# Kernel optimization log

Hardware: AMD Instinct MI355X
Metric: run time of the kernel (lower is better)

The kernel has to match this reference:

```python
import math
import jax
import jax.numpy as jnp
import numpy as np

NUM_TOKENS = 8192
MODEL_DIM = 2048
NUM_EXPERTS = 64
CAPACITY_FACTOR = 1.0


def setup_inputs() -> dict:
    key = jax.random.key(0)
    k1, k2 = jax.random.split(key)
    x = jax.random.normal(k1, (NUM_TOKENS, MODEL_DIM), dtype=jnp.float32)
    # gate weight, torch Linear layout [num_experts, model_dim]
    wg = jax.random.normal(k2, (NUM_EXPERTS, MODEL_DIM), dtype=jnp.float32) / np.sqrt(MODEL_DIM).astype(np.float32)
    return {"x": x, "wg": wg}


def top2gating(logits, capacity_factor):
    s, e = logits.shape  # static under jit
    capacity = int(math.ceil(2 * s / e * capacity_factor))
    gates = jax.nn.softmax(logits, axis=1)  # [s, e]

    # top-1 expert
    indices1_s = jnp.argmax(gates, axis=1)
    mask1 = jax.nn.one_hot(indices1_s, e, dtype=jnp.int32)  # [s, e]

    # top-2 expert via gumbel-perturbed logits with expert-1 masked out
    gumbel = jax.random.gumbel(jax.random.key(42), logits.shape, dtype=logits.dtype)
    logits_w_noise = logits + gumbel
    logits_except1 = jnp.where(mask1.astype(bool), -jnp.inf, logits_w_noise)
    indices2_s = jnp.argmax(logits_except1, axis=1)
    mask2 = jax.nn.one_hot(indices2_s, e, dtype=jnp.int32)

    # positions within each expert's buffer (prefix sums over tokens)
    locations1 = jnp.cumsum(mask1, axis=0) - 1  # [s, e]
    locations2 = jnp.cumsum(mask2, axis=0) - 1
    locations2 = locations2 + jnp.sum(mask1, axis=0, keepdims=True)

    # load-balancing aux loss
    me = jnp.mean(gates, axis=0)
    ce = jnp.mean(mask1.astype(gates.dtype), axis=0)
    l_aux = jnp.mean(me * ce) * (e * e)

    # drop tokens beyond capacity
    mask1 = mask1 * (locations1 < capacity).astype(jnp.int32)
    mask2 = mask2 * (locations2 < capacity).astype(jnp.int32)

    locations1_s = jnp.sum(locations1 * mask1, axis=1)  # [s]
    locations2_s = jnp.sum(locations2 * mask2, axis=1)

    mask1_f = mask1.astype(gates.dtype)
    mask2_f = mask2.astype(gates.dtype)
    gates1_s = jnp.sum(gates * mask1_f, axis=1)  # [s]
    gates2_s = jnp.sum(gates * mask2_f, axis=1)
    denom_s = jnp.maximum(gates1_s + gates2_s, jnp.finfo(gates.dtype).eps)
    gates1_s = gates1_s / denom_s
    gates2_s = gates2_s / denom_s

    gates1 = gates1_s[:, None] * mask1_f  # [s, e]
    gates2 = gates2_s[:, None] * mask2_f

    locations1_sc = jax.nn.one_hot(locations1_s, capacity, dtype=gates.dtype)  # [s, c]
    locations2_sc = jax.nn.one_hot(locations2_s, capacity, dtype=gates.dtype)

    combine_weights = (gates1[:, :, None] * locations1_sc[:, None, :]
                       + gates2[:, :, None] * locations2_sc[:, None, :])  # [s, e, c]
    dispatch_mask = combine_weights.astype(bool)
    return l_aux, combine_weights, dispatch_mask


def reference(x, wg):
    logits = x @ wg.T  # [s, e]
    return top2gating(logits, CAPACITY_FACTOR)
```

## Files before the change

### kernel.cpp

```cpp
#include <hip/hip_runtime.h>
#include <hip/hip_bf16.h>
#include <stdint.h>

#define TOKENS 8192
#define DIM 2048
#define EXPERTS 64
#define CAP 256
#define COMB_ELEMS ((size_t)TOKENS * EXPERTS * CAP)
#define OUT_ELEMS (1 + 2 * COMB_ELEMS)

__device__ __forceinline__ void tf_round(uint32_t& a, uint32_t& b, int r) {
  a += b;
  b = (b << r) | (b >> (32 - r));
  b ^= a;
}

__device__ __forceinline__ void threefry2x32(uint32_t k0, uint32_t k1,
                                             uint32_t x0, uint32_t x1,
                                             uint32_t& o0, uint32_t& o1) {
  const uint32_t ks0 = k0, ks1 = k1, ks2 = k0 ^ k1 ^ 0x1BD11BDAu;
  x0 += ks0; x1 += ks1;
  tf_round(x0, x1, 13); tf_round(x0, x1, 15); tf_round(x0, x1, 26); tf_round(x0, x1, 6);
  x0 += ks1; x1 += ks2 + 1u;
  tf_round(x0, x1, 17); tf_round(x0, x1, 29); tf_round(x0, x1, 16); tf_round(x0, x1, 24);
  x0 += ks2; x1 += ks0 + 2u;
  tf_round(x0, x1, 13); tf_round(x0, x1, 15); tf_round(x0, x1, 26); tf_round(x0, x1, 6);
  x0 += ks0; x1 += ks1 + 3u;
  tf_round(x0, x1, 17); tf_round(x0, x1, 29); tf_round(x0, x1, 16); tf_round(x0, x1, 24);
  x0 += ks1; x1 += ks2 + 4u;
  tf_round(x0, x1, 13); tf_round(x0, x1, 15); tf_round(x0, x1, 26); tf_round(x0, x1, 6);
  x0 += ks2; x1 += ks0 + 5u;
  o0 = x0; o1 = x1;
}

__global__ __launch_bounds__(256) void k_zero(float* __restrict__ out) {
  const size_t n4 = OUT_ELEMS / 4;
  float4* o4 = reinterpret_cast<float4*>(out);
  size_t i = (size_t)blockIdx.x * blockDim.x + threadIdx.x;
  const size_t stride = (size_t)gridDim.x * blockDim.x;
  const float4 z = make_float4(0.f, 0.f, 0.f, 0.f);
  for (; i < n4; i += stride) o4[i] = z;
  if (blockIdx.x == 0 && threadIdx.x == 0) out[2 * COMB_ELEMS] = 0.f;
}

__global__ __launch_bounds__(256) void k_logits(const float* __restrict__ x,
                                                const float* __restrict__ wg,
                                                float* __restrict__ logits) {
  __shared__ float xs[32][33];
  __shared__ float wt[32][64];
  const int tid = threadIdx.x;
  const int tok0 = blockIdx.x * 32;
  const int e0 = (tid & 15) * 4;
  const int t0 = (tid >> 4) * 2;

  const int xr = tid >> 3;
  const int xc = (tid & 7) << 2;
  const int wr = tid >> 2;
  const int wc = (tid & 3) << 3;

  const float* xp = x + (size_t)(tok0 + xr) * DIM + xc;
  const float* wp = wg + (size_t)wr * DIM + wc;

  float4 xv  = *reinterpret_cast<const float4*>(xp);
  float4 wv0 = *reinterpret_cast<const float4*>(wp);
  float4 wv1 = *reinterpret_cast<const float4*>(wp + 4);

  float acc[2][4] = {{0.f, 0.f, 0.f, 0.f}, {0.f, 0.f, 0.f, 0.f}};

  for (int k0 = 0; k0 < DIM; k0 += 32) {
    *reinterpret_cast<float4*>(&xs[xr][xc]) = xv;
    wt[wc + 0][wr] = wv0.x; wt[wc + 1][wr] = wv0.y;
    wt[wc + 2][wr] = wv0.z; wt[wc + 3][wr] = wv0.w;
    wt[wc + 4][wr] = wv1.x; wt[wc + 5][wr] = wv1.y;
    wt[wc + 6][wr] = wv1.z; wt[wc + 7][wr] = wv1.w;
    __syncthreads();
    if (k0 + 32 < DIM) {
      xv  = *reinterpret_cast<const float4*>(xp + k0 + 32);
      wv0 = *reinterpret_cast<const float4*>(wp + k0 + 32);
      wv1 = *reinterpret_cast<const float4*>(wp + k0 + 36);
    }
#pragma unroll
    for (int kk = 0; kk < 32; ++kk) {
      const float4 b = *reinterpret_cast<const float4*>(&wt[kk][e0]);
      const float a0 = xs[t0][kk];
      const float a1 = xs[t0 + 1][kk];
      acc[0][0] = fmaf(a0, b.x, acc[0][0]);
      acc[0][1] = fmaf(a0, b.y, acc[0][1]);
      acc[0][2] = fmaf(a0, b.z, acc[0][2]);
      acc[0][3] = fmaf(a0, b.w, acc[0][3]);
      acc[1][0] = fmaf(a1, b.x, acc[1][0]);
      acc[1][1] = fmaf(a1, b.y, acc[1][1]);
      acc[1][2] = fmaf(a1, b.z, acc[1][2]);
      acc[1][3] = fmaf(a1, b.w, acc[1][3]);
    }
    __syncthreads();
  }
#pragma unroll
  for (int i = 0; i < 2; ++i) {
    float4 r = make_float4(acc[i][0], acc[i][1], acc[i][2], acc[i][3]);
    *reinterpret_cast<float4*>(&logits[(size_t)(tok0 + t0 + i) * EXPERTS + e0]) = r;
  }
}

__global__ __launch_bounds__(256) void k_gate(const float* __restrict__ logits,
    float* __restrict__ gates, int* __restrict__ e1, int* __restrict__ e2,
    float* __restrict__ g1, float* __restrict__ g2) {
  const int lane = threadIdx.x & 63;
  const int t = blockIdx.x * 4 + (threadIdx.x >> 6);
  const float logit = logits[(size_t)t * EXPERTS + lane];

  float m = logit;
#pragma unroll
  for (int off = 32; off > 0; off >>= 1) m = fmaxf(m, __shfl_xor(m, off));
  const float ex = expf(logit - m);
  float s = ex;
#pragma unroll
  for (int off = 32; off > 0; off >>= 1) s += __shfl_xor(s, off);
  const float gate = ex / s;
  gates[(size_t)t * EXPERTS + lane] = gate;

  float v1 = logit; int i1 = lane;
#pragma unroll
  for (int off = 32; off > 0; off >>= 1) {
    const float ov = __shfl_xor(v1, off);
    const int oi = __shfl_xor(i1, off);
    if (ov > v1 || (ov == v1 && oi < i1)) { v1 = ov; i1 = oi; }
  }

  const uint32_t i_flat = (uint32_t)t * 64u + (uint32_t)lane;
  uint32_t b0, b1;
  threefry2x32(0u, 42u, 0u, i_flat, b0, b1);
  const uint32_t bits = b0 ^ b1;
  float u = __uint_as_float((bits >> 9) | 0x3f800000u) - 1.0f;
  u += 1.17549435e-38f;
  const float gum = -logf(-logf(u));
  const float noisy = (lane == i1) ? -__builtin_inff() : (logit + gum);

  float v2 = noisy; int i2 = lane;
#pragma unroll
  for (int off = 32; off > 0; off >>= 1) {
    const float ov = __shfl_xor(v2, off);
    const int oi = __shfl_xor(i2, off);
    if (ov > v2 || (ov == v2 && oi < i2)) { v2 = ov; i2 = oi; }
  }

  const float gate1 = __shfl(gate, i1);
  const float gate2 = __shfl(gate, i2);
  if (lane == 0) { e1[t] = i1; e2[t] = i2; g1[t] = gate1; g2[t] = gate2; }
}

__global__ __launch_bounds__(256) void k_scan(const int* __restrict__ e1,
    const int* __restrict__ e2, const float* __restrict__ gates,
    int* __restrict__ loc1, int* __restrict__ loc2,
    int* __restrict__ counts1, float* __restrict__ gsum) {
  const int e = blockIdx.x;
  const int tid = threadIdx.x;
  const int lane = tid & 63;
  const int w = tid >> 6;
  __shared__ int wt4[4];
  __shared__ int carry;
  __shared__ float gw[4];
  if (tid == 0) carry = 0;

  float gs = 0.f;
  for (int base = 0; base < TOKENS; base += 256) {
    const int t = base + tid;
    const int p = (e1[t] == e) ? 1 : 0;
    gs += gates[(size_t)t * EXPERTS + e];
    const uint64_t mask = __ballot(p);
    const int rk = __popcll(mask & ((1ull << lane) - 1ull));
    if (lane == 0) wt4[w] = __popcll(mask);
    __syncthreads();
    int pre = carry;
#pragma unroll
    for (int i = 0; i < 4; ++i)
      if (i < w) pre += wt4[i];
    if (p) loc1[t] = pre + rk;
    const int tot = wt4[0] + wt4[1] + wt4[2] + wt4[3];
    __syncthreads();
    if (tid == 0) carry += tot;
  }
  __syncthreads();
  if (tid == 0) counts1[e] = carry;
  for (int base = 0; base < TOKENS; base += 256) {
    const int t = base + tid;
    const int p = (e2[t] == e) ? 1 : 0;
    const uint64_t mask = __ballot(p);
    const int rk = __popcll(mask & ((1ull << lane) - 1ull));
    if (lane == 0) wt4[w] = __popcll(mask);
    __syncthreads();
    int pre = carry;
#pragma unroll
    for (int i = 0; i < 4; ++i)
      if (i < w) pre += wt4[i];
    if (p) loc2[t] = pre + rk;
    const int tot = wt4[0] + wt4[1] + wt4[2] + wt4[3];
    __syncthreads();
    if (tid == 0) carry += tot;
  }
#pragma unroll
  for (int off = 32; off > 0; off >>= 1) gs += __shfl_xor(gs, off);
  if (lane == 0) gw[w] = gs;
  __syncthreads();
  if (tid == 0) gsum[e] = gw[0] + gw[1] + gw[2] + gw[3];
}

__global__ void k_laux(const float* __restrict__ gsum, const int* __restrict__ counts1,
                       float* __restrict__ out) {
  const int lane = threadIdx.x;
  float v = gsum[lane] * (float)counts1[lane];
#pragma unroll
  for (int off = 32; off > 0; off >>= 1) v += __shfl_xor(v, off);
  if (lane == 0) out[0] = v * (1.0f / 1048576.0f);
}

__global__ __launch_bounds__(256) void k_scatter(const int* __restrict__ e1,
    const int* __restrict__ e2, const float* __restrict__ g1,
    const float* __restrict__ g2, const int* __restrict__ loc1,
    const int* __restrict__ loc2, float* __restrict__ out) {
  const int t = blockIdx.x * 256 + threadIdx.x;
  const int a = e1[t], b = e2[t];
  const int l1 = loc1[t], l2 = loc2[t];
  const bool k1 = l1 < CAP;
  const bool k2 = l2 < CAP;
  const float ga = k1 ? g1[t] : 0.f;
  const float gb = k2 ? g2[t] : 0.f;
  const float denom = fmaxf(ga + gb, 1.1920929e-07f);
  float* __restrict__ combine = out + 1;
  float* __restrict__ dispatch = out + 1 + COMB_ELEMS;
  if (k1) {
    const size_t idx = ((size_t)t * EXPERTS + a) * CAP + l1;
    combine[idx] = ga / denom;
    dispatch[idx] = 1.0f;
  }
  if (k2) {
    const size_t idx = ((size_t)t * EXPERTS + b) * CAP + l2;
    combine[idx] = gb / denom;
    dispatch[idx] = 1.0f;
  }
}

extern "C" void kernel_launch(void* const* d_in, const int* in_sizes, int n_in,
                              void* d_out, int out_size, void* d_ws, size_t ws_size,
                              hipStream_t stream) {
  const float* x = (const float*)d_in[0];
  const float* wg = (const float*)d_in[1];
  float* out = (float*)d_out;

  float* ws = (float*)d_ws;
  float* logits  = ws;
  float* gates   = ws + 524288;
  int*   e1      = (int*)(ws + 1048576);
  int*   e2      = e1 + TOKENS;
  int*   loc1    = e2 + TOKENS;
  int*   loc2    = loc1 + TOKENS;
  int*   counts1 = loc2 + TOKENS;
  float* g1      = (float*)(counts1 + 64);
  float* g2      = g1 + TOKENS;
  float* gsum    = g2 + TOKENS;

  k_zero<<<2048, 256, 0, stream>>>(out);
  k_logits<<<TOKENS / 32, 256, 0, stream>>>(x, wg, logits);
  k_gate<<<TOKENS / 4, 256, 0, stream>>>(logits, gates, e1, e2, g1, g2);
  k_scan<<<EXPERTS, 256, 0, stream>>>(e1, e2, gates, loc1, loc2, counts1, gsum);
  k_laux<<<1, 64, 0, stream>>>(gsum, counts1, out);
  k_scatter<<<TOKENS / 256, 256, 0, stream>>>(e1, e2, g1, g2, loc1, loc2, out);
}
```

Baseline: 1.214 ms.

## Fuse zero-fill, gate GEMM and softmax/top2 into one kernel with partial gate sums

Merges the output zeroing, logits GEMM and gating into a single launch. Extra blocks do the zero-fill alongside the GEMM blocks, and the GEMM blocks run softmax, top-2 selection and Gumbel noise directly from logits kept in shared memory. Per-block column sums of the gates replace the full gates buffer that the scan kernel used to re-read. The aux-loss kernel is folded into the scatter kernel. This removes launches and the logits/gates round trips through global memory. The trade-off is that GEMM and zero-fill blocks now compete for bandwidth, and the zero-fill of roughly 1 GB of output still dominates.

```diff
diff --git a/kernel.cpp b/kernel.cpp
--- a/kernel.cpp
+++ b/kernel.cpp
@@ -8,6 +8,9 @@
 #define CAP 256
 #define COMB_ELEMS ((size_t)TOKENS * EXPERTS * CAP)
 #define OUT_ELEMS (1 + 2 * COMB_ELEMS)
+
+#define GEMM_BLOCKS 256
+#define ZERO_BLOCKS 2048
 
 __device__ __forceinline__ void tf_round(uint32_t& a, uint32_t& b, int r) {
   a += b;
@@ -33,22 +36,30 @@
   o0 = x0; o1 = x1;
 }
 
-__global__ __launch_bounds__(256) void k_zero(float* __restrict__ out) {
-  const size_t n4 = OUT_ELEMS / 4;
-  float4* o4 = reinterpret_cast<float4*>(out);
-  size_t i = (size_t)blockIdx.x * blockDim.x + threadIdx.x;
-  const size_t stride = (size_t)gridDim.x * blockDim.x;
-  const float4 z = make_float4(0.f, 0.f, 0.f, 0.f);
-  for (; i < n4; i += stride) o4[i] = z;
-  if (blockIdx.x == 0 && threadIdx.x == 0) out[2 * COMB_ELEMS] = 0.f;
-}
-
-__global__ __launch_bounds__(256) void k_logits(const float* __restrict__ x,
-                                                const float* __restrict__ wg,
-                                                float* __restrict__ logits) {
+__global__ __launch_bounds__(256) void k_fused(const float* __restrict__ x,
+                                               const float* __restrict__ wg,
+                                               float* __restrict__ out,
+                                               int* __restrict__ e1, int* __restrict__ e2,
+                                               float* __restrict__ g1, float* __restrict__ g2,
+                                               float* __restrict__ gpart) {
   __shared__ float xs[32][33];
   __shared__ float wt[32][64];
+  __shared__ float gpl[4][64];
+
   const int tid = threadIdx.x;
+
+  if (blockIdx.x >= GEMM_BLOCKS) {
+    const size_t n4 = OUT_ELEMS / 4;
+    float4* o4 = reinterpret_cast<float4*>(out);
+    const int zb = blockIdx.x - GEMM_BLOCKS;
+    size_t i = (size_t)zb * 256 + tid;
+    const size_t stride = (size_t)ZERO_BLOCKS * 256;
+    const float4 z = make_float4(0.f, 0.f, 0.f, 0.f);
+    for (; i < n4; i += stride) o4[i] = z;
+    if (zb == 0 && tid == 0) out[2 * COMB_ELEMS] = 0.f;
+    return;
+  }
+
   const int tok0 = blockIdx.x * 32;
   const int e0 = (tid & 15) * 4;
   const int t0 = (tid >> 4) * 2;
@@ -95,62 +106,68 @@
     }
     __syncthreads();
   }
-#pragma unroll
-  for (int i = 0; i < 2; ++i) {
-    float4 r = make_float4(acc[i][0], acc[i][1], acc[i][2], acc[i][3]);
-    *reinterpret_cast<float4*>(&logits[(size_t)(tok0 + t0 + i) * EXPERTS + e0]) = r;
-  }
-}
-
-__global__ __launch_bounds__(256) void k_gate(const float* __restrict__ logits,
-    float* __restrict__ gates, int* __restrict__ e1, int* __restrict__ e2,
-    float* __restrict__ g1, float* __restrict__ g2) {
-  const int lane = threadIdx.x & 63;
-  const int t = blockIdx.x * 4 + (threadIdx.x >> 6);
-  const float logit = logits[(size_t)t * EXPERTS + lane];
-
-  float m = logit;
-#pragma unroll
-  for (int off = 32; off > 0; off >>= 1) m = fmaxf(m, __shfl_xor(m, off));
-  const float ex = expf(logit - m);
-  float s = ex;
-#pragma unroll
-  for (int off = 32; off > 0; off >>= 1) s += __shfl_xor(s, off);
-  const float gate = ex / s;
-  gates[(size_t)t * EXPERTS + lane] = gate;
-
-  float v1 = logit; int i1 = lane;
-#pragma unroll
-  for (int off = 32; off > 0; off >>= 1) {
-    const float ov = __shfl_xor(v1, off);
-    const int oi = __shfl_xor(i1, off);
-    if (ov > v1 || (ov == v1 && oi < i1)) { v1 = ov; i1 = oi; }
-  }
-
-  const uint32_t i_flat = (uint32_t)t * 64u + (uint32_t)lane;
-  uint32_t b0, b1;
-  threefry2x32(0u, 42u, 0u, i_flat, b0, b1);
-  const uint32_t bits = b0 ^ b1;
-  float u = __uint_as_float((bits >> 9) | 0x3f800000u) - 1.0f;
-  u += 1.17549435e-38f;
-  const float gum = -logf(-logf(u));
-  const float noisy = (lane == i1) ? -__builtin_inff() : (logit + gum);
-
-  float v2 = noisy; int i2 = lane;
-#pragma unroll
-  for (int off = 32; off > 0; off >>= 1) {
-    const float ov = __shfl_xor(v2, off);
-    const int oi = __shfl_xor(i2, off);
-    if (ov > v2 || (ov == v2 && oi < i2)) { v2 = ov; i2 = oi; }
-  }
-
-  const float gate1 = __shfl(gate, i1);
-  const float gate2 = __shfl(gate, i2);
-  if (lane == 0) { e1[t] = i1; e2[t] = i2; g1[t] = gate1; g2[t] = gate2; }
+
+#pragma unroll
+  for (int i = 0; i < 2; ++i)
+    *reinterpret_cast<float4*>(&wt[t0 + i][e0]) =
+        make_float4(acc[i][0], acc[i][1], acc[i][2], acc[i][3]);
+  __syncthreads();
+
+  const int w = tid >> 6;
+  const int lane = tid & 63;
+  float colsum = 0.f;
+  for (int lt = w * 8; lt < w * 8 + 8; ++lt) {
+    const int t = tok0 + lt;
+    const float logit = wt[lt][lane];
+
+    float m = logit;
+#pragma unroll
+    for (int off = 32; off > 0; off >>= 1) m = fmaxf(m, __shfl_xor(m, off));
+    const float ex = expf(logit - m);
+    float s = ex;
+#pragma unroll
+    for (int off = 32; off > 0; off >>= 1) s += __shfl_xor(s, off);
+    const float gate = ex / s;
+    colsum += gate;
+
+    float v1 = logit; int i1 = lane;
+#pragma unroll
+    for (int off = 32; off > 0; off >>= 1) {
+      const float ov = __shfl_xor(v1, off);
+      const int oi = __shfl_xor(i1, off);
+      if (ov > v1 || (ov == v1 && oi < i1)) { v1 = ov; i1 = oi; }
+    }
+
+    const uint32_t i_flat = (uint32_t)t * 64u + (uint32_t)lane;
+    uint32_t b0, b1;
+    threefry2x32(0u, 42u, 0u, i_flat, b0, b1);
+    const uint32_t bits = b0 ^ b1;
+    float u = __uint_as_float((bits >> 9) | 0x3f800000u) - 1.0f;
+    u += 1.17549435e-38f;
+    const float gum = -logf(-logf(u));
+    const float noisy = (lane == i1) ? -__builtin_inff() : (logit + gum);
+
+    float v2 = noisy; int i2 = lane;
+#pragma unroll
+    for (int off = 32; off > 0; off >>= 1) {
+      const float ov = __shfl_xor(v2, off);
+      const int oi = __shfl_xor(i2, off);
+      if (ov > v2 || (ov == v2 && oi < i2)) { v2 = ov; i2 = oi; }
+    }
+
+    const float gate1 = __shfl(gate, i1);
+    const float gate2 = __shfl(gate, i2);
+    if (lane == 0) { e1[t] = i1; e2[t] = i2; g1[t] = gate1; g2[t] = gate2; }
+  }
+  gpl[w][lane] = colsum;
+  __syncthreads();
+  if (w == 0)
+    gpart[(size_t)blockIdx.x * 64 + lane] =
+        (gpl[0][lane] + gpl[1][lane]) + (gpl[2][lane] + gpl[3][lane]);
 }
 
 __global__ __launch_bounds__(256) void k_scan(const int* __restrict__ e1,
-    const int* __restrict__ e2, const float* __restrict__ gates,
+    const int* __restrict__ e2, const float* __restrict__ gpart,
     int* __restrict__ loc1, int* __restrict__ loc2,
     int* __restrict__ counts1, float* __restrict__ gsum) {
   const int e = blockIdx.x;
@@ -162,11 +179,16 @@
   __shared__ float gw[4];
   if (tid == 0) carry = 0;
 
-  float gs = 0.f;
+  float gp = gpart[(size_t)tid * 64 + e];
+#pragma unroll
+  for (int off = 32; off > 0; off >>= 1) gp += __shfl_xor(gp, off);
+  if (lane == 0) gw[w] = gp;
+  __syncthreads();
+  if (tid == 0) gsum[e] = (gw[0] + gw[1]) + (gw[2] + gw[3]);
+
   for (int base = 0; base < TOKENS; base += 256) {
     const int t = base + tid;
     const int p = (e1[t] == e) ? 1 : 0;
-    gs += gates[(size_t)t * EXPERTS + e];
     const uint64_t mask = __ballot(p);
     const int rk = __popcll(mask & ((1ull << lane) - 1ull));
     if (lane == 0) wt4[w] = __popcll(mask);
@@ -198,27 +220,21 @@
     __syncthreads();
     if (tid == 0) carry += tot;
   }
-#pragma unroll
-  for (int off = 32; off > 0; off >>= 1) gs += __shfl_xor(gs, off);
-  if (lane == 0) gw[w] = gs;
-  __syncthreads();
-  if (tid == 0) gsum[e] = gw[0] + gw[1] + gw[2] + gw[3];
-}
-
-__global__ void k_laux(const float* __restrict__ gsum, const int* __restrict__ counts1,
-                       float* __restrict__ out) {
-  const int lane = threadIdx.x;
-  float v = gsum[lane] * (float)counts1[lane];
-#pragma unroll
-  for (int off = 32; off > 0; off >>= 1) v += __shfl_xor(v, off);
-  if (lane == 0) out[0] = v * (1.0f / 1048576.0f);
 }
 
 __global__ __launch_bounds__(256) void k_scatter(const int* __restrict__ e1,
     const int* __restrict__ e2, const float* __restrict__ g1,
     const float* __restrict__ g2, const int* __restrict__ loc1,
-    const int* __restrict__ loc2, float* __restrict__ out) {
-  const int t = blockIdx.x * 256 + threadIdx.x;
+    const int* __restrict__ loc2, const float* __restrict__ gsum,
+    const int* __restrict__ counts1, float* __restrict__ out) {
+  const int tid = threadIdx.x;
+  if (blockIdx.x == 0 && tid < 64) {
+    float v = gsum[tid] * (float)counts1[tid];
+#pragma unroll
+    for (int off = 32; off > 0; off >>= 1) v += __shfl_xor(v, off);
+    if (tid == 0) out[0] = v * (1.0f / 1048576.0f);
+  }
+  const int t = blockIdx.x * 256 + tid;
   const int a = e1[t], b = e2[t];
   const int l1 = loc1[t], l2 = loc2[t];
   const bool k1 = l1 < CAP;
@@ -247,10 +263,7 @@
   const float* wg = (const float*)d_in[1];
   float* out = (float*)d_out;
 
-  float* ws = (float*)d_ws;
-  float* logits  = ws;
-  float* gates   = ws + 524288;
-  int*   e1      = (int*)(ws + 1048576);
+  int*   e1      = (int*)d_ws;
   int*   e2      = e1 + TOKENS;
   int*   loc1    = e2 + TOKENS;
   int*   loc2    = loc1 + TOKENS;
@@ -258,11 +271,9 @@
   float* g1      = (float*)(counts1 + 64);
   float* g2      = g1 + TOKENS;
   float* gsum    = g2 + TOKENS;
-
-  k_zero<<<2048, 256, 0, stream>>>(out);
-  k_logits<<<TOKENS / 32, 256, 0, stream>>>(x, wg, logits);
-  k_gate<<<TOKENS / 4, 256, 0, stream>>>(logits, gates, e1, e2, g1, g2);
-  k_scan<<<EXPERTS, 256, 0, stream>>>(e1, e2, gates, loc1, loc2, counts1, gsum);
-  k_laux<<<1, 64, 0, stream>>>(gsum, counts1, out);
-  k_scatter<<<TOKENS / 256, 256, 0, stream>>>(e1, e2, g1, g2, loc1, loc2, out);
-}
+  float* gpart   = gsum + 64;
+
+  k_fused<<<GEMM_BLOCKS + ZERO_BLOCKS, 256, 0, stream>>>(x, wg, out, e1, e2, g1, g2, gpart);
+  k_scan<<<EXPERTS, 256, 0, stream>>>(e1, e2, gpart, loc1, loc2, counts1, gsum);
+  k_scatter<<<TOKENS / 256, 256, 0, stream>>>(e1, e2, g1, g2, loc1, loc2, gsum, counts1, out);
+}
```

Result: faster. 1.143 ms (-5.9%).
